# Kernel tuning notes

Measured on AMD Instinct MI355X. Metric: run time of the kernel, lower is better.

Reference implementation:

```python
import jax, jax.numpy as jnp
import numpy as np
from jax import lax

T, D, H = 8192, 2048, 256  # seq_len, feature dim, lstm hidden (= D/8)


def _lstm(x, W, U, b, reverse=False):
    """Keras LSTM with activation='sigmoid', recurrent_activation='sigmoid'.
    x: (T, Din); W: (Din, 4H); U: (H, 4H); b: (4H,). Gate order i,f,c,o."""
    if reverse:
        x = x[::-1]
    zx = x @ W + b  # precompute input projection for all timesteps: (T, 4H)
    h0 = jnp.zeros((U.shape[0],), x.dtype)

    def step(carry, z):
        h, c = carry
        z = z + h @ U
        i, f, g, o = jnp.split(z, 4)
        c = jax.nn.sigmoid(f) * c + jax.nn.sigmoid(i) * jax.nn.sigmoid(g)
        h = jax.nn.sigmoid(o) * jax.nn.sigmoid(c)
        return (h, c), h

    _, hs = lax.scan(step, (h0, h0), zx)
    return hs[::-1] if reverse else hs


def _bilstm(x, Wf, Uf, bf, Wb, Ub, bb):
    # Bidirectional merge_mode='concat'
    return jnp.concatenate(
        [_lstm(x, Wf, Uf, bf), _lstm(x, Wb, Ub, bb, reverse=True)], axis=-1)


def setup_inputs() -> dict:
    key = jax.random.key(0)
    ks = jax.random.split(key, 13)
    s = 0.02
    f32 = jnp.float32
    return {
        "x": jax.random.normal(ks[0], (T, D), f32),
        "W1f": s * jax.random.normal(ks[1], (D, 4 * H), f32),
        "U1f": s * jax.random.normal(ks[2], (H, 4 * H), f32),
        "b1f": jnp.zeros((4 * H,), f32),
        "W1b": s * jax.random.normal(ks[3], (D, 4 * H), f32),
        "U1b": s * jax.random.normal(ks[4], (H, 4 * H), f32),
        "b1b": jnp.zeros((4 * H,), f32),
        "W2f": s * jax.random.normal(ks[5], (2 * H, 4 * H), f32),
        "U2f": s * jax.random.normal(ks[6], (H, 4 * H), f32),
        "b2f": jnp.zeros((4 * H,), f32),
        "W2b": s * jax.random.normal(ks[7], (2 * H, 4 * H), f32),
        "U2b": s * jax.random.normal(ks[8], (H, 4 * H), f32),
        "b2b": jnp.zeros((4 * H,), f32),
    }


def reference(x, W1f, U1f, b1f, W1b, U1b, b1b,
              W2f, U2f, b2f, W2b, U2b, b2b):
    M1 = _bilstm(x, W1f, U1f, b1f, W1b, U1b, b1b)    # (T, 2H) = (T, D/4)
    M2 = _bilstm(M1, W2f, U2f, b2f, W2b, U2b, b2b)   # (T, D/4)
    temp1 = jnp.concatenate([x, M1], axis=1)          # (T, 5D/4)
    temp2 = jnp.concatenate([x, M2], axis=1)          # (T, 5D/4)
    return jnp.stack([temp1, temp2], axis=0)          # (2, T, 5D/4)
```

## Files before the change

kernel.cpp:

```cpp
#include <hip/hip_runtime.h>
#include <stdint.h>

#define T_STEPS 8192
#define DIN     2048
#define NH      256
#define G4      1024
#define OUTW    2560

__device__ __forceinline__ float sigf(float x) {
    return 1.0f / (1.0f + __expf(-x));
}

__device__ __forceinline__ int dot4(int a, int b, int c) {
#if __has_builtin(__builtin_amdgcn_sdot4)
    return __builtin_amdgcn_sdot4(a, b, c, false);
#else
    int r = c;
#pragma unroll
    for (int i = 0; i < 4; ++i) {
        int ai = (a << (24 - 8 * i)) >> 24;
        int bi = (b << (24 - 8 * i)) >> 24;
        r += ai * bi;
    }
    return r;
#endif
}

__global__ void quant_u_kernel(const float* __restrict__ U0, const float* __restrict__ U1,
                               const float* __restrict__ U2, const float* __restrict__ U3,
                               uint32_t* __restrict__ uq, float* __restrict__ sc) {
    const float* U = (blockIdx.x == 0) ? U0 : (blockIdx.x == 1) ? U1
                   : (blockIdx.x == 2) ? U2 : U3;
    uint32_t* uqo = uq + (size_t)blockIdx.x * (NH / 4) * G4;
    float* sco = sc + (size_t)blockIdx.x * G4;

    int j = threadIdx.x;
    float ma = 0.f;
    for (int k = 0; k < NH; ++k) ma = fmaxf(ma, fabsf(U[(size_t)k * G4 + j]));
    float inv = (ma > 0.f) ? 127.f / ma : 0.f;
    sco[j] = ma * (1.0f / (127.f * 127.f));
    for (int w = 0; w < NH / 4; ++w) {
        uint32_t word = 0;
#pragma unroll
        for (int b = 0; b < 4; ++b) {
            float v = U[(size_t)(4 * w + b) * G4 + j];
            int q = __float2int_rn(v * inv);
            q = max(-127, min(127, q));
            word |= ((uint32_t)(q & 0xff)) << (8 * b);
        }
        uqo[(size_t)w * G4 + j] = word;
    }
}

__global__ void copy_x_kernel(const float4* __restrict__ x4, float* __restrict__ out) {
    const int total = 2 * T_STEPS * (DIN / 4);
    for (int i = blockIdx.x * blockDim.x + threadIdx.x; i < total;
         i += gridDim.x * blockDim.x) {
        int o   = i >> 22;
        int rem = i & ((1 << 22) - 1);
        int t   = rem >> 9;
        int c4  = rem & 511;
        float4 v = x4[(size_t)t * 512 + c4];
        *(float4*)(out + (size_t)o * T_STEPS * OUTW + (size_t)t * OUTW + (size_t)c4 * 4) = v;
    }
}

__global__ __launch_bounds__(256) void gemm_zx_kernel(
    const float* __restrict__ A, int lda,
    const float* __restrict__ B, const float* __restrict__ bias,
    float* __restrict__ C, int K) {
    __shared__ float As[64][17];
    __shared__ float Bs[16][68];
    int tid = threadIdx.x;
    int bm = blockIdx.y * 64, bn = blockIdx.x * 64;
    int trow = tid >> 4, tcol = tid & 15;
    int ar = tid >> 2, ac = (tid & 3) * 4;
    int br = tid >> 4, bc = (tid & 15) * 4;
    float acc[4][4] = {};

    for (int k0 = 0; k0 < K; k0 += 16) {
        float4 av = *(const float4*)(A + (size_t)(bm + ar) * lda + k0 + ac);
        float4 bv = *(const float4*)(B + (size_t)(k0 + br) * G4 + bn + bc);
        As[ar][ac + 0] = av.x; As[ar][ac + 1] = av.y;
        As[ar][ac + 2] = av.z; As[ar][ac + 3] = av.w;
        Bs[br][bc + 0] = bv.x; Bs[br][bc + 1] = bv.y;
        Bs[br][bc + 2] = bv.z; Bs[br][bc + 3] = bv.w;
        __syncthreads();
#pragma unroll
        for (int kk = 0; kk < 16; ++kk) {
            float af[4], bf[4];
#pragma unroll
            for (int i = 0; i < 4; ++i) af[i] = As[trow * 4 + i][kk];
#pragma unroll
            for (int i = 0; i < 4; ++i) bf[i] = Bs[kk][tcol * 4 + i];
#pragma unroll
            for (int i = 0; i < 4; ++i)
#pragma unroll
                for (int j = 0; j < 4; ++j)
                    acc[i][j] = fmaf(af[i], bf[j], acc[i][j]);
        }
        __syncthreads();
    }
#pragma unroll
    for (int i = 0; i < 4; ++i) {
        float4 v;
        v.x = acc[i][0] + bias[bn + tcol * 4 + 0];
        v.y = acc[i][1] + bias[bn + tcol * 4 + 1];
        v.z = acc[i][2] + bias[bn + tcol * 4 + 2];
        v.w = acc[i][3] + bias[bn + tcol * 4 + 3];
        *(float4*)(C + (size_t)(bm + trow * 4 + i) * G4 + bn + tcol * 4) = v;
    }
}

__global__ __attribute__((amdgpu_flat_work_group_size(1024, 1024)))
__attribute__((amdgpu_waves_per_eu(4, 4))) void lstm_scan_kernel(
    const float* __restrict__ Zxf, const float* __restrict__ Zxb,
    const uint32_t* __restrict__ Uqf, const uint32_t* __restrict__ Uqb,
    const float* __restrict__ scf, const float* __restrict__ scb,
    float* __restrict__ outbase) {
    __shared__ float s_lds[G4];
    __shared__ int4 hq_lds4[16];

    const int dir = blockIdx.x;
    const float* Zx = dir ? Zxb : Zxf;
    const uint32_t* Uq = dir ? Uqb : Uqf;
    const float* sc = dir ? scb : scf;

    const int j = threadIdx.x;

    int u[64];
#pragma unroll
    for (int w = 0; w < 64; ++w) u[w] = (int)Uq[(size_t)w * G4 + j];
#pragma unroll
    for (int w = 0; w < 64; w += 4)
        asm volatile("" : "+v"(u[w]), "+v"(u[w + 1]), "+v"(u[w + 2]), "+v"(u[w + 3]));

    const float scj = sc[j];

    if (j < 16) hq_lds4[j] = make_int4(0, 0, 0, 0);
    float c = 0.f;

    const int step = dir ? -1 : 1;
    const int t0 = dir ? (T_STEPS - 1) : 0;
    float zx0 = Zx[(size_t)t0 * G4 + j];
    float zx1 = Zx[(size_t)(t0 + step) * G4 + j];
    float* outp = outbase + 2048 + dir * NH;
    __syncthreads();

    int t = t0;
    for (int s = 0; s < T_STEPS; ++s) {
        int t2 = t + 2 * step;
        t2 = (t2 < 0) ? 0 : (t2 >= T_STEPS ? T_STEPS - 1 : t2);
        const float zx2 = Zx[(size_t)t2 * G4 + j];

        int acc = 0;
#pragma unroll
        for (int w4 = 0; w4 < 16; ++w4) {
            const int4 hw = hq_lds4[w4];
            acc = dot4(u[4 * w4 + 0], hw.x, acc);
            acc = dot4(u[4 * w4 + 1], hw.y, acc);
            acc = dot4(u[4 * w4 + 2], hw.z, acc);
            acc = dot4(u[4 * w4 + 3], hw.w, acc);
        }
        s_lds[j] = sigf(zx0 + (float)acc * scj);
        __syncthreads();

        if (j < NH) {
            float si = s_lds[j];
            float sf = s_lds[j + NH];
            float sg = s_lds[j + 2 * NH];
            float so = s_lds[j + 3 * NH];
            c = sf * c + si * sg;
            float h = so * sigf(c);
            outp[(size_t)t * OUTW + j] = h;
            int q = __float2int_rn(h * 127.f);
            q = max(0, min(127, q));
            ((uint8_t*)hq_lds4)[j] = (uint8_t)q;
        }
        __syncthreads();

        zx0 = zx1; zx1 = zx2;
        t += step;
    }
}

extern "C" void kernel_launch(void* const* d_in, const int* in_sizes, int n_in,
                              void* d_out, int out_size, void* d_ws, size_t ws_size,
                              hipStream_t stream) {
    const float* x   = (const float*)d_in[0];
    const float* W1f = (const float*)d_in[1];
    const float* U1f = (const float*)d_in[2];
    const float* b1f = (const float*)d_in[3];
    const float* W1b = (const float*)d_in[4];
    const float* U1b = (const float*)d_in[5];
    const float* b1b = (const float*)d_in[6];
    const float* W2f = (const float*)d_in[7];
    const float* U2f = (const float*)d_in[8];
    const float* b2f = (const float*)d_in[9];
    const float* W2b = (const float*)d_in[10];
    const float* U2b = (const float*)d_in[11];
    const float* b2b = (const float*)d_in[12];

    float* out  = (float*)d_out;
    float* out1 = out + (size_t)T_STEPS * OUTW;

    float* Zxf = (float*)d_ws;
    float* Zxb = Zxf + (size_t)T_STEPS * G4;
    uint32_t* uq = (uint32_t*)(Zxb + (size_t)T_STEPS * G4);
    float* scq = (float*)(uq + (size_t)4 * 64 * G4);

    quant_u_kernel<<<4, 1024, 0, stream>>>(U1f, U1b, U2f, U2b, uq, scq);
    copy_x_kernel<<<2048, 256, 0, stream>>>((const float4*)x, out);

    dim3 gg(16, 128);
    gemm_zx_kernel<<<gg, 256, 0, stream>>>(x, DIN, W1f, b1f, Zxf, DIN);
    gemm_zx_kernel<<<gg, 256, 0, stream>>>(x, DIN, W1b, b1b, Zxb, DIN);

    lstm_scan_kernel<<<2, 1024, 0, stream>>>(Zxf, Zxb,
                                             uq + (size_t)0 * 64 * G4, uq + (size_t)1 * 64 * G4,
                                             scq + 0 * G4, scq + 1 * G4, out);

    gemm_zx_kernel<<<gg, 256, 0, stream>>>(out + 2048, OUTW, W2f, b2f, Zxf, 512);
    gemm_zx_kernel<<<gg, 256, 0, stream>>>(out + 2048, OUTW, W2b, b2b, Zxb, 512);

    lstm_scan_kernel<<<2, 1024, 0, stream>>>(Zxf, Zxb,
                                             uq + (size_t)2 * 64 * G4, uq + (size_t)3 * 64 * G4,
                                             scq + 2 * G4, scq + 3 * G4, out1);
}
```

Before: 18.24 ms.

## Halve LSTM scan block size, two gate columns per thread with int4 weight layout

The recurrent scan kernel now runs 512 threads per block, and each thread computes two gate columns (j and j+512), holding 128 packed int8 weight words in registers. The quantised U layout is interleaved so each thread loads its weights as int4 vectors. The LDS broadcast of h is shared across two dot-product chains. This cuts waves per barrier and per-step synchronisation cost, at the price of double the per-thread serial dot work and higher register pressure.

```diff
diff --git a/kernel.cpp b/kernel.cpp
--- a/kernel.cpp
+++ b/kernel.cpp
@@ -48,7 +48,7 @@
             q = max(-127, min(127, q));
             word |= ((uint32_t)(q & 0xff)) << (8 * b);
         }
-        uqo[(size_t)w * G4 + j] = word;
+        uqo[(size_t)(w >> 2) * G4 * 4 + (size_t)j * 4 + (w & 3)] = word;
     }
 }
 
@@ -112,8 +112,8 @@
     }
 }
 
-__global__ __attribute__((amdgpu_flat_work_group_size(1024, 1024)))
-__attribute__((amdgpu_waves_per_eu(4, 4))) void lstm_scan_kernel(
+__global__ __attribute__((amdgpu_flat_work_group_size(512, 512)))
+__attribute__((amdgpu_waves_per_eu(2, 2))) void lstm_scan_kernel(
     const float* __restrict__ Zxf, const float* __restrict__ Zxb,
     const uint32_t* __restrict__ Uqf, const uint32_t* __restrict__ Uqb,
     const float* __restrict__ scf, const float* __restrict__ scb,
@@ -126,24 +126,37 @@
     const uint32_t* Uq = dir ? Uqb : Uqf;
     const float* sc = dir ? scb : scf;
 
-    const int j = threadIdx.x;
-
-    int u[64];
-#pragma unroll
-    for (int w = 0; w < 64; ++w) u[w] = (int)Uq[(size_t)w * G4 + j];
-#pragma unroll
-    for (int w = 0; w < 64; w += 4)
-        asm volatile("" : "+v"(u[w]), "+v"(u[w + 1]), "+v"(u[w + 2]), "+v"(u[w + 3]));
-
-    const float scj = sc[j];
+    const int j  = threadIdx.x;
+    const int j2 = threadIdx.x + 512;
+
+    const int4* Uq4 = (const int4*)Uq;
+    int4 a0 = Uq4[0 * G4 + j],  a1 = Uq4[1 * G4 + j],  a2 = Uq4[2 * G4 + j],  a3 = Uq4[3 * G4 + j];
+    int4 a4 = Uq4[4 * G4 + j],  a5 = Uq4[5 * G4 + j],  a6 = Uq4[6 * G4 + j],  a7 = Uq4[7 * G4 + j];
+    int4 a8 = Uq4[8 * G4 + j],  a9 = Uq4[9 * G4 + j],  a10 = Uq4[10 * G4 + j], a11 = Uq4[11 * G4 + j];
+    int4 a12 = Uq4[12 * G4 + j], a13 = Uq4[13 * G4 + j], a14 = Uq4[14 * G4 + j], a15 = Uq4[15 * G4 + j];
+    int4 b0 = Uq4[0 * G4 + j2],  b1 = Uq4[1 * G4 + j2],  b2 = Uq4[2 * G4 + j2],  b3 = Uq4[3 * G4 + j2];
+    int4 b4 = Uq4[4 * G4 + j2],  b5 = Uq4[5 * G4 + j2],  b6 = Uq4[6 * G4 + j2],  b7 = Uq4[7 * G4 + j2];
+    int4 b8 = Uq4[8 * G4 + j2],  b9 = Uq4[9 * G4 + j2],  b10 = Uq4[10 * G4 + j2], b11 = Uq4[11 * G4 + j2];
+    int4 b12 = Uq4[12 * G4 + j2], b13 = Uq4[13 * G4 + j2], b14 = Uq4[14 * G4 + j2], b15 = Uq4[15 * G4 + j2];
+#define PIN4(v) asm volatile("" : "+v"(v.x), "+v"(v.y), "+v"(v.z), "+v"(v.w))
+    PIN4(a0); PIN4(a1); PIN4(a2); PIN4(a3); PIN4(a4); PIN4(a5); PIN4(a6); PIN4(a7);
+    PIN4(a8); PIN4(a9); PIN4(a10); PIN4(a11); PIN4(a12); PIN4(a13); PIN4(a14); PIN4(a15);
+    PIN4(b0); PIN4(b1); PIN4(b2); PIN4(b3); PIN4(b4); PIN4(b5); PIN4(b6); PIN4(b7);
+    PIN4(b8); PIN4(b9); PIN4(b10); PIN4(b11); PIN4(b12); PIN4(b13); PIN4(b14); PIN4(b15);
+#undef PIN4
+
+    const float sca = sc[j];
+    const float scb2 = sc[j2];
 
     if (j < 16) hq_lds4[j] = make_int4(0, 0, 0, 0);
     float c = 0.f;
 
     const int step = dir ? -1 : 1;
     const int t0 = dir ? (T_STEPS - 1) : 0;
-    float zx0 = Zx[(size_t)t0 * G4 + j];
-    float zx1 = Zx[(size_t)(t0 + step) * G4 + j];
+    float zxa0 = Zx[(size_t)t0 * G4 + j];
+    float zxb0 = Zx[(size_t)t0 * G4 + j2];
+    float zxa1 = Zx[(size_t)(t0 + step) * G4 + j];
+    float zxb1 = Zx[(size_t)(t0 + step) * G4 + j2];
     float* outp = outbase + 2048 + dir * NH;
     __syncthreads();
 
@@ -151,18 +164,27 @@
     for (int s = 0; s < T_STEPS; ++s) {
         int t2 = t + 2 * step;
         t2 = (t2 < 0) ? 0 : (t2 >= T_STEPS ? T_STEPS - 1 : t2);
-        const float zx2 = Zx[(size_t)t2 * G4 + j];
-
-        int acc = 0;
-#pragma unroll
-        for (int w4 = 0; w4 < 16; ++w4) {
-            const int4 hw = hq_lds4[w4];
-            acc = dot4(u[4 * w4 + 0], hw.x, acc);
-            acc = dot4(u[4 * w4 + 1], hw.y, acc);
-            acc = dot4(u[4 * w4 + 2], hw.z, acc);
-            acc = dot4(u[4 * w4 + 3], hw.w, acc);
-        }
-        s_lds[j] = sigf(zx0 + (float)acc * scj);
+        const float zxa2 = Zx[(size_t)t2 * G4 + j];
+        const float zxb2 = Zx[(size_t)t2 * G4 + j2];
+
+        int acca = 0, accb = 0;
+#define DOTS2(UA, UB, HM) do { const int4 hh = (HM);                        \
+            acca = dot4((UA).x, hh.x, acca); accb = dot4((UB).x, hh.x, accb); \
+            acca = dot4((UA).y, hh.y, acca); accb = dot4((UB).y, hh.y, accb); \
+            acca = dot4((UA).z, hh.z, acca); accb = dot4((UB).z, hh.z, accb); \
+            acca = dot4((UA).w, hh.w, acca); accb = dot4((UB).w, hh.w, accb); } while (0)
+        DOTS2(a0, b0, hq_lds4[0]);   DOTS2(a1, b1, hq_lds4[1]);
+        DOTS2(a2, b2, hq_lds4[2]);   DOTS2(a3, b3, hq_lds4[3]);
+        DOTS2(a4, b4, hq_lds4[4]);   DOTS2(a5, b5, hq_lds4[5]);
+        DOTS2(a6, b6, hq_lds4[6]);   DOTS2(a7, b7, hq_lds4[7]);
+        DOTS2(a8, b8, hq_lds4[8]);   DOTS2(a9, b9, hq_lds4[9]);
+        DOTS2(a10, b10, hq_lds4[10]); DOTS2(a11, b11, hq_lds4[11]);
+        DOTS2(a12, b12, hq_lds4[12]); DOTS2(a13, b13, hq_lds4[13]);
+        DOTS2(a14, b14, hq_lds4[14]); DOTS2(a15, b15, hq_lds4[15]);
+#undef DOTS2
+
+        s_lds[j]  = sigf(zxa0 + (float)acca * sca);
+        s_lds[j2] = sigf(zxb0 + (float)accb * scb2);
         __syncthreads();
 
         if (j < NH) {
@@ -179,7 +201,8 @@
         }
         __syncthreads();
 
-        zx0 = zx1; zx1 = zx2;
+        zxa0 = zxa1; zxa1 = zxa2;
+        zxb0 = zxb1; zxb1 = zxb2;
         t += step;
     }
 }
@@ -216,14 +239,14 @@
     gemm_zx_kernel<<<gg, 256, 0, stream>>>(x, DIN, W1f, b1f, Zxf, DIN);
     gemm_zx_kernel<<<gg, 256, 0, stream>>>(x, DIN, W1b, b1b, Zxb, DIN);
 
-    lstm_scan_kernel<<<2, 1024, 0, stream>>>(Zxf, Zxb,
-                                             uq + (size_t)0 * 64 * G4, uq + (size_t)1 * 64 * G4,
-                                             scq + 0 * G4, scq + 1 * G4, out);
+    lstm_scan_kernel<<<2, 512, 0, stream>>>(Zxf, Zxb,
+                                            uq + (size_t)0 * 64 * G4, uq + (size_t)1 * 64 * G4,
+                                            scq + 0 * G4, scq + 1 * G4, out);
 
     gemm_zx_kernel<<<gg, 256, 0, stream>>>(out + 2048, OUTW, W2f, b2f, Zxf, 512);
     gemm_zx_kernel<<<gg, 256, 0, stream>>>(out + 2048, OUTW, W2b, b2b, Zxb, 512);
 
-    lstm_scan_kernel<<<2, 1024, 0, stream>>>(Zxf, Zxb,
-                                             uq + (size_t)2 * 64 * G4, uq + (size_t)3 * 64 * G4,
-                                             scq + 2 * G4, scq + 3 * G4, out1);
-}
+    lstm_scan_kernel<<<2, 512, 0, stream>>>(Zxf, Zxb,
+                                            uq + (size_t)2 * 64 * G4, uq + (size_t)3 * 64 * G4,
+                                            scq + 2 * G4, scq + 3 * G4, out1);
+}
```

Result: faster. 16.28 ms (-10.8%).
